# Performance work log

Measured on AMD Instinct MI355X. Metric: run time of the kernel, lower is better.

Reference implementation:

```python
import jax, jax.numpy as jnp
import numpy as np

V = 25426          # tgt_vocab_size
D = 256            # d_model
H = 8              # heads
DH = 2048          # dim_head (d_ff passed positionally as d_head in source)
INNER = H * DH     # 16384
CLS = V            # cls token id (same value for t1 and t2 in source)
MASK_TOK = V + 2   # mask token id
VT = V + 3         # total embedding vocab


def _pos_encoding(n, d):
    pos = np.arange(n, dtype=np.float32)[:, None]
    div = np.exp(np.arange(0, d, 2, dtype=np.float32) * (-np.log(10000.0) / d))
    pe = np.zeros((n, d), dtype=np.float32)
    pe[:, 0::2] = np.sin(pos * div)
    pe[:, 1::2] = np.cos(pos * div)
    return jnp.asarray(pe)


def _layernorm(x, g, b, eps=1e-5):
    m = x.mean(-1, keepdims=True)
    v = ((x - m) ** 2).mean(-1, keepdims=True)
    return (x - m) / jnp.sqrt(v + eps) * g + b


def _cross_attn(x, ctx, pad_mask, Wq, Wk, Wv, Wo, bo):
    # x: [B,N,D], ctx: [B,M,Dc], pad_mask: [B,M] True = masked
    B, N, _ = x.shape
    M = ctx.shape[1]
    scale = DH ** -0.5
    q = (x @ Wq).reshape(B, N, H, DH)
    k = (ctx @ Wk).reshape(B, M, H, DH)
    v = (ctx @ Wv).reshape(B, M, H, DH)
    sim = jnp.einsum('bihd,bjhd->bhij', q, k) * scale  # [B,H,N,M]
    neg = -jnp.finfo(sim.dtype).max
    sim = jnp.where(pad_mask[:, None, None, :], neg, sim)
    attn = jax.nn.softmax(sim, axis=-1)
    out = jnp.einsum('bhij,bjhd->bihd', attn, v).reshape(B, N, INNER)
    return out @ Wo + bo


def _decoder(x, tgt_pad, src_mask, enc_output, p):
    a = _cross_attn(x, x, tgt_pad, p['Wq_s'], p['Wk_s'], p['Wv_s'], p['Wo_s'], p['bo_s'])
    x = _layernorm(x + a, p['g1'], p['be1'])
    a = _cross_attn(x, enc_output, src_mask, p['Wq_c'], p['Wk_c'], p['Wv_c'], p['Wo_c'], p['bo_c'])
    x = _layernorm(x + a, p['g2'], p['be2'])
    f = jax.nn.gelu(x @ p['W1'] + p['b1'], approximate=False) @ p['W2'] + p['b2']
    x = _layernorm(x + f, p['g3'], p['be3'])
    return x


def setup_inputs() -> dict:
    key = jax.random.key(0)
    ks = jax.random.split(key, 32)
    B, S, L = 2, 1024, 767
    d = {
        'src_input_id': jax.random.randint(ks[0], (B, S), 0, V),
        'tgt_input_id_t1': jax.random.randint(ks[1], (B, L), 0, V),
        'tgt_input_id_t2': jax.random.randint(ks[2], (B, L), 0, V),
        'original_lens': jax.random.randint(ks[3], (B,), 1, L),
        'enc_output': jax.random.normal(ks[4], (B, S, D), dtype=jnp.float32),
    }
    emb = jax.random.normal(ks[5], (VT, D), dtype=jnp.float32) * 0.02
    d['token_emb'] = emb.at[0].set(0.0)  # padding_idx=0
    s = 0.02
    d['Wq_s'] = jax.random.normal(ks[6], (D, INNER)) * s
    d['Wk_s'] = jax.random.normal(ks[7], (D, INNER)) * s
    d['Wv_s'] = jax.random.normal(ks[8], (D, INNER)) * s
    d['Wo_s'] = jax.random.normal(ks[9], (INNER, D)) * s
    d['bo_s'] = jnp.zeros((D,), jnp.float32)
    d['Wq_c'] = jax.random.normal(ks[10], (D, INNER)) * s
    d['Wk_c'] = jax.random.normal(ks[11], (D, INNER)) * s
    d['Wv_c'] = jax.random.normal(ks[12], (D, INNER)) * s
    d['Wo_c'] = jax.random.normal(ks[13], (INNER, D)) * s
    d['bo_c'] = jnp.zeros((D,), jnp.float32)
    d['W1'] = jax.random.normal(ks[14], (D, D)) * s  # Mlp hidden collapses to D (source bug)
    d['b1'] = jnp.zeros((D,), jnp.float32)
    d['W2'] = jax.random.normal(ks[15], (D, D)) * s
    d['b2'] = jnp.zeros((D,), jnp.float32)
    for i, n in enumerate(['g1', 'g2', 'g3']):
        d[n] = jnp.ones((D,), jnp.float32)
    for n in ['be1', 'be2', 'be3']:
        d[n] = jnp.zeros((D,), jnp.float32)
    d['Wfc'] = jax.random.normal(ks[16], (D, V)) * s
    d['bfc'] = jnp.zeros((V,), jnp.float32)
    return d


def reference(src_input_id, tgt_input_id_t1, tgt_input_id_t2, original_lens,
              enc_output, token_emb,
              Wq_s, Wk_s, Wv_s, Wo_s, bo_s,
              Wq_c, Wk_c, Wv_c, Wo_c, bo_c,
              W1, b1, W2, b2, g1, be1, g2, be2, g3, be3, Wfc, bfc):
    p = dict(Wq_s=Wq_s, Wk_s=Wk_s, Wv_s=Wv_s, Wo_s=Wo_s, bo_s=bo_s,
             Wq_c=Wq_c, Wk_c=Wk_c, Wv_c=Wv_c, Wo_c=Wo_c, bo_c=bo_c,
             W1=W1, b1=b1, W2=W2, b2=b2, g1=g1, be1=be1, g2=g2, be2=be2, g3=g3, be3=be3)
    B = tgt_input_id_t1.shape[0]
    cls = jnp.full((B, 1), CLS, dtype=tgt_input_id_t1.dtype)
    t1 = jnp.concatenate([cls, tgt_input_id_t1], axis=1)
    t2 = jnp.concatenate([cls, tgt_input_id_t2], axis=1)
    tgt = jnp.concatenate([t1, t2], axis=1)          # [B, T]
    tgt_pad = tgt == 0
    src_mask = src_input_id == 0
    # generate=True path: mask positions where id==mask_token or id==0
    tgt_mask = (tgt == MASK_TOK) | (tgt == 0)
    tgt_ids = jnp.where(tgt_mask, MASK_TOK, tgt)
    x = token_emb[tgt_ids]                            # [B, T, D]
    pe = _pos_encoding(x.shape[1], D)
    x = 2.0 * x + pe[None, :, :]                      # prepare_tokens: x + (x + pe), faithful to source
    x = _decoder(x, tgt_pad, src_mask, enc_output, p)
    logits = x @ Wfc + bfc
    return logits[:, 1:, :], x[:, 0, :]
```

## Files before the change

### kernel.cpp

```cpp
#include <hip/hip_runtime.h>
#include <hip/hip_bf16.h>
#include <float.h>
#include <math.h>

#define BB 2
#define SS 1024
#define LL 767
#define TT 1536
#define DD 256
#define HH 8
#define DHD 2048
#define INNER_ 16384
#define VV 25426
#define VPAD 25472
#define CLS_TOK 25426
#define MASK_TOKEN 25428
#define ROWS (BB*TT)
#define SROWS (BB*SS)

typedef __attribute__((ext_vector_type(8))) __bf16 bf16x8;
typedef __attribute__((ext_vector_type(4))) float f32x4;

__device__ __forceinline__ unsigned short f2bu(float f) {
    union { float f; unsigned u; } v; v.f = f;
    unsigned r = v.u + 0x7fff + ((v.u >> 16) & 1);
    return (unsigned short)(r >> 16);
}
__device__ __forceinline__ float bu2f(unsigned short u) {
    union { unsigned u; float f; } v; v.u = ((unsigned)u) << 16;
    return v.f;
}

__device__ __forceinline__ void gload16(const void* g, void* l) {
    __builtin_amdgcn_global_load_lds(
        (const __attribute__((address_space(1))) void*)g,
        (__attribute__((address_space(3))) void*)l, 16, 0, 0);
}


__global__ __launch_bounds__(256) void embed_kernel(
    const int* __restrict__ t1, const int* __restrict__ t2,
    const float* __restrict__ emb, float* __restrict__ x,
    unsigned short* __restrict__ xb, unsigned char* __restrict__ tgt_pad)
{
    int t = blockIdx.x, b = blockIdx.y, d = threadIdx.x;
    int raw;
    if (t == 0)            raw = CLS_TOK;
    else if (t <= LL)      raw = t1[b * LL + (t - 1)];
    else if (t == LL + 1)  raw = CLS_TOK;
    else                   raw = t2[b * LL + (t - LL - 2)];
    int id = (raw == 0 || raw == MASK_TOKEN) ? MASK_TOKEN : raw;
    int i = d >> 1;
    float ang = (float)t * expf(-0.03597789208f * (float)(2 * i));
    float pe = (d & 1) ? cosf(ang) : sinf(ang);
    float val = 2.f * emb[(long long)id * DD + d] + pe;
    long long idx = ((long long)(b * TT + t)) * DD + d;
    x[idx] = val;
    xb[idx] = f2bu(val);
    if (d == 0) tgt_pad[b * TT + t] = (raw == 0) ? 1 : 0;
}

__global__ __launch_bounds__(256) void masks_kernel(
    const int* __restrict__ src, unsigned char* __restrict__ m, int* __restrict__ rm)
{
    int i = blockIdx.x * 256 + threadIdx.x;
    if (i < SROWS) m[i] = (src[i] == 0) ? 1 : 0;
    if (i < ROWS) {
        int b = i / TT, t = i % TT;
        rm[i] = (t == 0) ? -1 : (b * (TT - 1) + t - 1);
    }
}

__global__ __launch_bounds__(256) void copycls_kernel(
    const float* __restrict__ x, float* __restrict__ out2)
{
    int b = blockIdx.x, d = threadIdx.x;
    out2[b * DD + d] = x[(long long)b * TT * DD + d];
}

__global__ __launch_bounds__(256) void conv_bf16v4(
    const float* __restrict__ in, unsigned short* __restrict__ out)
{
    size_t i = ((size_t)blockIdx.x * 256 + threadIdx.x) * 4;
    float4 v = *reinterpret_cast<const float4*>(in + i);
    ushort4 u;
    u.x = f2bu(v.x); u.y = f2bu(v.y); u.z = f2bu(v.z); u.w = f2bu(v.w);
    *reinterpret_cast<ushort4*>(out + i) = u;
}

__global__ __launch_bounds__(256) void convW6(
    const float* __restrict__ w0, const float* __restrict__ w1,
    const float* __restrict__ w2, const float* __restrict__ w3,
    const float* __restrict__ w4, const float* __restrict__ w5,
    unsigned short* __restrict__ dst)
{
    int seg = blockIdx.y;
    const float* s = seg == 0 ? w0 : seg == 1 ? w1 : seg == 2 ? w2 :
                     seg == 3 ? w3 : seg == 4 ? w4 : w5;
    size_t i = ((size_t)blockIdx.x * 256 + threadIdx.x) * 4;
    float4 v = *reinterpret_cast<const float4*>(s + i);
    ushort4 u;
    u.x = f2bu(v.x); u.y = f2bu(v.y); u.z = f2bu(v.z); u.w = f2bu(v.w);
    *reinterpret_cast<ushort4*>(dst + (size_t)seg * ((size_t)DD * INNER_) + i) = u;
}

__global__ __launch_bounds__(256) void transpose_conv(
    const float* __restrict__ in, unsigned short* __restrict__ out,
    int R, int Cin, int Nout)
{
    __shared__ float t[32][33];
    int k0 = blockIdx.x * 32, n0 = blockIdx.y * 32;
#pragma unroll
    for (int i = 0; i < 4; ++i) {
        int k = k0 + threadIdx.y + i * 8;
        int n = n0 + threadIdx.x;
        t[threadIdx.y + i * 8][threadIdx.x] = (n < Cin) ? in[(size_t)k * Cin + n] : 0.f;
    }
    __syncthreads();
#pragma unroll
    for (int i = 0; i < 4; ++i) {
        int n = n0 + threadIdx.y + i * 8;
        int k = k0 + threadIdx.x;
        out[(size_t)n * R + k] = f2bu(t[threadIdx.x][threadIdx.y + i * 8]);
    }
}

template<int STORE, int SPLITK>
__global__ __launch_bounds__(256) void gemm_bt(
    const unsigned short* __restrict__ A, int lda,
    const unsigned short* __restrict__ B, int ldb,
    void* __restrict__ Cv, int ldc,
    int M, int N, int K, float alpha, int zs,
    long long sAb, long long sAh, long long sBb, long long sBh,
    long long sCb, long long sCh,
    const float* __restrict__ bias, const int* __restrict__ rowmap)
{
    __shared__ unsigned short As[8192];
    __shared__ unsigned short Bs[8192];
    const int tid = threadIdx.x;
    const int w = tid >> 6, l = tid & 63;
    const int m0 = blockIdx.x * 128, n0 = blockIdx.y * 128;

    int kbeg = 0, kend = K;
    long long czoff = 0;
    if (SPLITK > 1) {
        constexpr int KSH = (SPLITK == 8) ? 3 : (SPLITK == 4) ? 2 : (SPLITK == 2) ? 1 : 0;
        int kidx = blockIdx.z & (SPLITK - 1);
        int zr = blockIdx.z >> KSH;
        int zb = zr >> zs;
        int zh = zr - (zb << zs);
        int kc = K / SPLITK;
        kbeg = kidx * kc; kend = kbeg + kc;
        A += zb * sAb + zh * sAh;
        B += zb * sBb + zh * sBh;
        czoff = zb * sCb + zh * sCh;
    } else {
        int zb = blockIdx.z >> zs;
        int zh = blockIdx.z - (zb << zs);
        A += zb * sAb + zh * sAh;
        B += zb * sBb + zh * sBh;
        czoff = zb * sCb + zh * sCh;
    }

    const int wr = (w >> 1) << 6, wc = (w & 1) << 6;
    const int lrow = l & 15, lk = l >> 4;

    const int sro = (w << 3) + (l >> 3);
    const int sko = (((l & 7) ^ (l >> 3)) << 3);
    const int ldst = (w << 10) + (l << 4);

    f32x4 acc[4][4];
#pragma unroll
    for (int mi = 0; mi < 4; ++mi)
#pragma unroll
        for (int ni = 0; ni < 4; ++ni)
            acc[mi][ni] = (f32x4){0.f, 0.f, 0.f, 0.f};

    for (int kt = kbeg; kt < kend; kt += 64) {
#pragma unroll
        for (int j = 0; j < 4; ++j)
            gload16(A + (size_t)(m0 + sro + j * 32) * lda + kt + sko,
                    (char*)As + (j << 12) + ldst);
#pragma unroll
        for (int j = 0; j < 4; ++j)
            gload16(B + (size_t)(n0 + sro + j * 32) * ldb + kt + sko,
                    (char*)Bs + (j << 12) + ldst);
        __syncthreads();

#pragma unroll
        for (int kk = 0; kk < 2; ++kk) {
            const int slot = (kk << 2) + lk;
            bf16x8 af[4], bfr[4];
#pragma unroll
            for (int mi = 0; mi < 4; ++mi) {
                int ra = wr + (mi << 4) + lrow;
                af[mi] = *reinterpret_cast<const bf16x8*>(
                    (const char*)As + (ra << 7) + ((slot ^ (ra & 7)) << 4));
            }
#pragma unroll
            for (int ni = 0; ni < 4; ++ni) {
                int rb = wc + (ni << 4) + lrow;
                bfr[ni] = *reinterpret_cast<const bf16x8*>(
                    (const char*)Bs + (rb << 7) + ((slot ^ (rb & 7)) << 4));
            }
#pragma unroll
            for (int mi = 0; mi < 4; ++mi)
#pragma unroll
                for (int ni = 0; ni < 4; ++ni)
                    acc[mi][ni] = __builtin_amdgcn_mfma_f32_16x16x32_bf16(
                        af[mi], bfr[ni], acc[mi][ni], 0, 0, 0);
        }
        __syncthreads();
    }

    if (STORE == 0) {
        unsigned short* C = (unsigned short*)Cv + czoff;
#pragma unroll
        for (int mi = 0; mi < 4; ++mi) {
            int r = m0 + wr + (mi << 4) + (lk << 2);
#pragma unroll
            for (int ni = 0; ni < 4; ++ni) {
                int c = n0 + wc + (ni << 4) + lrow;
#pragma unroll
                for (int q = 0; q < 4; ++q)
                    C[(size_t)(r + q) * ldc + c] = f2bu(acc[mi][ni][q] * alpha);
            }
        }
    } else if (STORE == 1) {
        unsigned short* C = (unsigned short*)Cv + czoff;
#pragma unroll
        for (int ni = 0; ni < 4; ++ni) {
            int c = n0 + wc + (ni << 4) + lrow;
#pragma unroll
            for (int mi = 0; mi < 4; ++mi) {
                int r = m0 + wr + (mi << 4) + (lk << 2);
                ushort4 u;
                u.x = f2bu(acc[mi][ni][0] * alpha);
                u.y = f2bu(acc[mi][ni][1] * alpha);
                u.z = f2bu(acc[mi][ni][2] * alpha);
                u.w = f2bu(acc[mi][ni][3] * alpha);
                *reinterpret_cast<ushort4*>(&C[(size_t)c * ldc + r]) = u;
            }
        }
    } else if (STORE == 2) {
        float* C = (float*)Cv;
#pragma unroll
        for (int mi = 0; mi < 4; ++mi) {
            int r = m0 + wr + (mi << 4) + (lk << 2);
#pragma unroll
            for (int q = 0; q < 4; ++q) {
                int rm = rowmap[r + q];
                if (rm < 0) continue;
#pragma unroll
                for (int ni = 0; ni < 4; ++ni) {
                    int c = n0 + wc + (ni << 4) + lrow;
                    if (c < N) C[(size_t)rm * ldc + c] = acc[mi][ni][q] * alpha + bias[c];
                }
            }
        }
    } else if (STORE == 3) {
        float* C = (float*)Cv + czoff;
#pragma unroll
        for (int mi = 0; mi < 4; ++mi) {
            int r = m0 + wr + (mi << 4) + (lk << 2);
#pragma unroll
            for (int ni = 0; ni < 4; ++ni) {
                int c = n0 + wc + (ni << 4) + lrow;
#pragma unroll
                for (int q = 0; q < 4; ++q)
                    atomicAdd(&C[(size_t)(r + q) * ldc + c], acc[mi][ni][q] * alpha);
            }
        }
    } else if (STORE == 4) {
        unsigned short* C = (unsigned short*)Cv + czoff;
#pragma unroll
        for (int mi = 0; mi < 4; ++mi) {
            int r = m0 + wr + (mi << 4) + (lk << 2);
#pragma unroll
            for (int ni = 0; ni < 4; ++ni) {
                int c = n0 + wc + (ni << 4) + lrow;
#pragma unroll
                for (int q = 0; q < 4; ++q) {
                    float v = acc[mi][ni][q] * alpha + bias[c];
                    v = 0.5f * v * (1.f + erff(v * 0.70710678118f));
                    C[(size_t)(r + q) * ldc + c] = f2bu(v);
                }
            }
        }
    } else if (STORE == 5) {
        float* C = (float*)Cv + czoff;
#pragma unroll
        for (int mi = 0; mi < 4; ++mi) {
            int r = m0 + wr + (mi << 4) + (lk << 2);
#pragma unroll
            for (int ni = 0; ni < 4; ++ni) {
                int c = n0 + wc + (ni << 4) + lrow;
#pragma unroll
                for (int q = 0; q < 4; ++q)
                    C[(size_t)(r + q) * ldc + c] = acc[mi][ni][q] * alpha;
            }
        }
    } else if (STORE == 6) {
        unsigned short* C = (unsigned short*)Cv + czoff;
        const unsigned char* mrow =
            (const unsigned char*)rowmap + (size_t)(blockIdx.z >> zs) * N;
        float* rsum = (float*)bias;
        float rpart[4][4];
#pragma unroll
        for (int mi = 0; mi < 4; ++mi)
#pragma unroll
            for (int q = 0; q < 4; ++q) rpart[mi][q] = 0.f;
#pragma unroll
        for (int mi = 0; mi < 4; ++mi) {
            int r = m0 + wr + (mi << 4) + (lk << 2);
#pragma unroll
            for (int ni = 0; ni < 4; ++ni) {
                int c = n0 + wc + (ni << 4) + lrow;
                bool msk = mrow[c] != 0;
#pragma unroll
                for (int q = 0; q < 4; ++q) {
                    float e = msk ? 0.f : expf(acc[mi][ni][q] * alpha);
                    C[(size_t)(r + q) * ldc + c] = f2bu(e);
                    rpart[mi][q] += e;
                }
            }
        }
#pragma unroll
        for (int mi = 0; mi < 4; ++mi)
#pragma unroll
            for (int q = 0; q < 4; ++q) {
                float s = rpart[mi][q];
                s += __shfl_xor(s, 1);
                s += __shfl_xor(s, 2);
                s += __shfl_xor(s, 4);
                s += __shfl_xor(s, 8);
                if (lrow == 0) {
                    int r = m0 + wr + (mi << 4) + (lk << 2) + q;
                    atomicAdd(&rsum[(size_t)blockIdx.z * M + r], s);
                }
            }
    } else {
        float* C = (float*)Cv + czoff;
#pragma unroll
        for (int mi = 0; mi < 4; ++mi) {
            int r = m0 + wr + (mi << 4) + (lk << 2);
#pragma unroll
            for (int q = 0; q < 4; ++q) {
                float rinv = 1.f / bias[(size_t)blockIdx.z * M + r + q];
#pragma unroll
                for (int ni = 0; ni < 4; ++ni) {
                    int c = n0 + wc + (ni << 4) + lrow;
                    atomicAdd(&C[(size_t)(r + q) * ldc + c], acc[mi][ni][q] * rinv);
                }
            }
        }
    }
}

__global__ __launch_bounds__(256) void ln_kernel(
    float* __restrict__ x, const float* __restrict__ a,
    const float* __restrict__ abias,
    const float* __restrict__ g, const float* __restrict__ be,
    unsigned short* __restrict__ xb)
{
    __shared__ float red[4];
    const long long r = blockIdx.x;
    const int d = threadIdx.x;
    const long long idx = r * DD + d;
    float v = x[idx] + a[idx];
    if (abias) v += abias[d];

    float s = v;
#pragma unroll
    for (int off = 32; off > 0; off >>= 1) s += __shfl_down(s, off);
    if ((d & 63) == 0) red[d >> 6] = s;
    __syncthreads();
    float mean = (red[0] + red[1] + red[2] + red[3]) * (1.f / DD);
    __syncthreads();

    float df = v - mean;
    float s2 = df * df;
#pragma unroll
    for (int off = 32; off > 0; off >>= 1) s2 += __shfl_down(s2, off);
    if ((d & 63) == 0) red[d >> 6] = s2;
    __syncthreads();
    float var = (red[0] + red[1] + red[2] + red[3]) * (1.f / DD);

    float o = df / sqrtf(var + 1e-5f) * g[d] + be[d];
    x[idx] = o;
    xb[idx] = f2bu(o);
}

extern "C" void kernel_launch(void* const* d_in, const int* in_sizes, int n_in,
                              void* d_out, int out_size, void* d_ws, size_t ws_size,
                              hipStream_t stream)
{
    const int*   src_ids = (const int*)d_in[0];
    const int*   t1      = (const int*)d_in[1];
    const int*   t2      = (const int*)d_in[2];
    const float* enc  = (const float*)d_in[4];
    const float* emb  = (const float*)d_in[5];
    const float* Wq_s = (const float*)d_in[6];
    const float* Wk_s = (const float*)d_in[7];
    const float* Wv_s = (const float*)d_in[8];
    const float* Wo_s = (const float*)d_in[9];
    const float* bo_s = (const float*)d_in[10];
    const float* Wq_c = (const float*)d_in[11];
    const float* Wk_c = (const float*)d_in[12];
    const float* Wv_c = (const float*)d_in[13];
    const float* Wo_c = (const float*)d_in[14];
    const float* bo_c = (const float*)d_in[15];
    const float* W1   = (const float*)d_in[16];
    const float* b1   = (const float*)d_in[17];
    const float* W2   = (const float*)d_in[18];
    const float* b2   = (const float*)d_in[19];
    const float* g1   = (const float*)d_in[20];
    const float* g2v  = (const float*)d_in[21];
    const float* g3   = (const float*)d_in[22];
    const float* be1  = (const float*)d_in[23];
    const float* be2  = (const float*)d_in[24];
    const float* be3  = (const float*)d_in[25];
    const float* Wfc  = (const float*)d_in[26];
    const float* bfc  = (const float*)d_in[27];

    char* p = (char*)d_ws;
    float* x    = (float*)p;           p += (size_t)ROWS * DD * 4;
    float* aout = (float*)p;           p += (size_t)ROWS * DD * 4;
    float* rsum = (float*)p;           p += (size_t)16 * TT * 4;
    unsigned short* h1b  = (unsigned short*)p; p += (size_t)ROWS * DD * 2;
    unsigned short* xb   = (unsigned short*)p; p += (size_t)ROWS * DD * 2;
    unsigned short* encb = (unsigned short*)p; p += (size_t)SROWS * DD * 2;
    unsigned short* Wqb_s = (unsigned short*)p; p += (size_t)DD * INNER_ * 2;
    unsigned short* Wkb_s = (unsigned short*)p; p += (size_t)DD * INNER_ * 2;
    unsigned short* Wvb_s = (unsigned short*)p; p += (size_t)DD * INNER_ * 2;
    unsigned short* Wqb_c = (unsigned short*)p; p += (size_t)DD * INNER_ * 2;
    unsigned short* Wkb_c = (unsigned short*)p; p += (size_t)DD * INNER_ * 2;
    unsigned short* Wvb_c = (unsigned short*)p; p += (size_t)DD * INNER_ * 2;
    unsigned short* WoTs  = (unsigned short*)p; p += (size_t)DD * INNER_ * 2;
    unsigned short* WoTc  = (unsigned short*)p; p += (size_t)DD * INNER_ * 2;
    unsigned short* WfcT  = (unsigned short*)p; p += (size_t)VPAD * DD * 2;
    unsigned short* W1Tb  = (unsigned short*)p; p += (size_t)DD * DD * 2;
    unsigned short* W2Tb  = (unsigned short*)p; p += (size_t)DD * DD * 2;
    unsigned short* MtNb  = (unsigned short*)p; p += (size_t)4 * 524288 * 2;
    unsigned char* tgtpad = (unsigned char*)p; p += ROWS;
    unsigned char* srcpad = (unsigned char*)p; p += SROWS;
    p = (char*)(((size_t)p + 15) & ~(size_t)15);
    int* rowmap = (int*)p;             p += (size_t)ROWS * 4;

    unsigned short* Mtb_s = MtNb;
    unsigned short* Ntb_s = MtNb + 524288;
    unsigned short* Mtb_c = MtNb + 2 * 524288;
    unsigned short* Ntb_c = MtNb + 3 * 524288;

    unsigned short* ob = (unsigned short*)d_out;
    unsigned short* simS = ob;
    unsigned short* Pb   = ob + 37748736;
    unsigned short* YTb  = Pb + 6291456;
    float* MNacc = (float*)d_out;

    const size_t accset = (size_t)ROWS * DD * 4 + (size_t)16 * TT * 4;
    const long long WBLK = 4194304;

    embed_kernel<<<dim3(TT, BB), 256, 0, stream>>>(t1, t2, emb, x, xb, tgtpad);
    masks_kernel<<<dim3(ROWS / 256), 256, 0, stream>>>(src_ids, srcpad, rowmap);
    conv_bf16v4<<<dim3((SROWS * DD) / 1024), 256, 0, stream>>>(enc, encb);

    dim3 tcb(32, 8);
    convW6<<<dim3((DD * INNER_) / 1024, 6), 256, 0, stream>>>(
        Wq_s, Wk_s, Wv_s, Wq_c, Wk_c, Wv_c, Wqb_s);
    transpose_conv<<<dim3(512, 8), tcb, 0, stream>>>(Wo_s, WoTs, INNER_, DD, DD);
    transpose_conv<<<dim3(512, 8), tcb, 0, stream>>>(Wo_c, WoTc, INNER_, DD, DD);
    transpose_conv<<<dim3(8, VPAD / 32), tcb, 0, stream>>>(Wfc, WfcT, DD, VV, VPAD);
    transpose_conv<<<dim3(8, 8), tcb, 0, stream>>>(W1, W1Tb, DD, DD, DD);
    transpose_conv<<<dim3(8, 8), tcb, 0, stream>>>(W2, W2Tb, DD, DD, DD);

    const float scale = 0.022097086912079608f;
    const long long Z0 = 0;

    hipMemsetAsync(MNacc, 0, (size_t)4 * 524288 * 4, stream);
    gemm_bt<3, 4><<<dim3(2, 2, 64), 256, 0, stream>>>(
        Wkb_s, INNER_, Wqb_s, INNER_, MNacc, 256, 256, 256, DHD, 1.f, 3,
        3 * WBLK, 2048, 3 * WBLK, 2048, 2 * 524288, 65536, nullptr, nullptr);
    gemm_bt<3, 4><<<dim3(2, 2, 64), 256, 0, stream>>>(
        WoTs, INNER_, Wvb_s, INNER_, MNacc + 524288, 2048, 256, 256, DHD, 1.f, 3,
        WBLK, 2048, 3 * WBLK, 2048, 2 * 524288, 256, nullptr, nullptr);
    conv_bf16v4<<<dim3((4 * 524288) / 1024), 256, 0, stream>>>(MNacc, MtNb);

    hipMemsetAsync(aout, 0, accset, stream);
    gemm_bt<0, 1><<<dim3(24, 2, 8), 256, 0, stream>>>(
        xb, DD, Mtb_s, DD, Pb, DD, ROWS, DD, DD, 1.f, 3,
        Z0, Z0, Z0, 65536, Z0, 786432, nullptr, nullptr);
    gemm_bt<1, 1><<<dim3(24, 2, 8), 256, 0, stream>>>(
        xb, DD, Ntb_s, 2048, YTb, ROWS, ROWS, DD, DD, 1.f, 3,
        Z0, Z0, Z0, 256, Z0, 786432, nullptr, nullptr);
    gemm_bt<6, 1><<<dim3(12, 12, 16), 256, 0, stream>>>(
        Pb, DD, xb, DD, simS, TT, TT, TT, DD, scale, 3,
        393216, 786432, 393216, Z0,
        18874368, 2359296, (const float*)rsum, (const int*)tgtpad);
    gemm_bt<7, 1><<<dim3(12, 2, 16), 256, 0, stream>>>(
        simS, TT, YTb, ROWS, aout, DD, TT, DD, TT, 1.f, 3,
        18874368, 2359296, 1536, 786432,
        393216, Z0, rsum, nullptr);
    ln_kernel<<<dim3(ROWS), 256, 0, stream>>>(x, aout, bo_s, g1, be1, xb);

    hipMemsetAsync(aout, 0, accset, stream);
    gemm_bt<0, 1><<<dim3(24, 2, 8), 256, 0, stream>>>(
        xb, DD, Mtb_c, DD, Pb, DD, ROWS, DD, DD, 1.f, 3,
        Z0, Z0, Z0, 65536, Z0, 786432, nullptr, nullptr);
    gemm_bt<1, 1><<<dim3(16, 2, 8), 256, 0, stream>>>(
        encb, DD, Ntb_c, 2048, YTb, SROWS, SROWS, DD, DD, 1.f, 3,
        Z0, Z0, Z0, 256, Z0, 524288, nullptr, nullptr);
    gemm_bt<6, 1><<<dim3(12, 8, 16), 256, 0, stream>>>(
        Pb, DD, encb, DD, simS, SS, TT, SS, DD, scale, 3,
        393216, 786432, 262144, Z0,
        12582912, 1572864, (const float*)rsum, (const int*)srcpad);
    gemm_bt<7, 1><<<dim3(12, 2, 16), 256, 0, stream>>>(
        simS, SS, YTb, SROWS, aout, DD, TT, DD, SS, 1.f, 3,
        12582912, 1572864, 1024, 524288,
        393216, Z0, rsum, nullptr);
    ln_kernel<<<dim3(ROWS), 256, 0, stream>>>(x, aout, bo_c, g2v, be2, xb);

    gemm_bt<4, 1><<<dim3(24, 2, 1), 256, 0, stream>>>(
        xb, DD, W1Tb, DD, h1b, DD, ROWS, DD, DD, 1.f, 0,
        Z0, Z0, Z0, Z0, Z0, Z0, b1, nullptr);
    gemm_bt<5, 1><<<dim3(24, 2, 1), 256, 0, stream>>>(
        h1b, DD, W2Tb, DD, aout, DD, ROWS, DD, DD, 1.f, 0,
        Z0, Z0, Z0, Z0, Z0, Z0, nullptr, nullptr);
    ln_kernel<<<dim3(ROWS), 256, 0, stream>>>(x, aout, b2, g3, be3, xb);

    gemm_bt<2, 1><<<dim3(24, VPAD / 128, 1), 256, 0, stream>>>(
        xb, DD, WfcT, DD, d_out, VV, ROWS, VV, DD, 1.f, 0,
        Z0, Z0, Z0, Z0, Z0, Z0, bfc, rowmap);

    copycls_kernel<<<dim3(BB), 256, 0, stream>>>(
        x, (float*)d_out + (long long)BB * (TT - 1) * VV);
}
```

Baseline: 566.9 us.

## Fuse attention score, exp and value GEMMs into one flash-style kernel

Replaces the separate score GEMM (writing exp'd bf16 scores to global memory with atomic row sums) and the value GEMM (atomic float accumulation across heads) with a single kernel. It keeps the query tile in LDS, streams key/value tiles, computes unnormalized exp scores in LDS, and accumulates the output per head. Per-head outputs are written without atomics and summed in a new layernorm kernel, which removes the memsets and the large intermediate score tensor. Softmax still skips max subtraction, as before, and the kernel uses about 66KB of LDS per block. Its 384-block grid may underfill the GPU.

```diff
diff --git a/kernel.cpp b/kernel.cpp
--- a/kernel.cpp
+++ b/kernel.cpp
@@ -287,7 +287,7 @@
                 }
             }
         }
-    } else if (STORE == 5) {
+    } else {
         float* C = (float*)Cv + czoff;
 #pragma unroll
         for (int mi = 0; mi < 4; ++mi) {
@@ -300,61 +300,187 @@
                     C[(size_t)(r + q) * ldc + c] = acc[mi][ni][q] * alpha;
             }
         }
-    } else if (STORE == 6) {
-        unsigned short* C = (unsigned short*)Cv + czoff;
-        const unsigned char* mrow =
-            (const unsigned char*)rowmap + (size_t)(blockIdx.z >> zs) * N;
-        float* rsum = (float*)bias;
-        float rpart[4][4];
-#pragma unroll
-        for (int mi = 0; mi < 4; ++mi)
-#pragma unroll
-            for (int q = 0; q < 4; ++q) rpart[mi][q] = 0.f;
+    }
+}
+
+template<int KVT>
+__global__ __launch_bounds__(256) void attn_fused(
+    const unsigned short* __restrict__ P,
+    const unsigned short* __restrict__ KV,
+    const unsigned short* __restrict__ YT,
+    float* __restrict__ Oh,
+    const unsigned char* __restrict__ mask,
+    float scale)
+{
+    constexpr int kvtok = KVT * 64;
+    constexpr int ytld = BB * kvtok;
+    __shared__ unsigned short Pq[64 * 256];
+    __shared__ unsigned short Stg[64 * 256];
+    __shared__ unsigned short Sc[64 * 64];
+    __shared__ float rs[64];
+
+    const int tid = threadIdx.x;
+    const int w = tid >> 6, l = tid & 63;
+    const int lrow = l & 15, lk = l >> 4;
+    const int q0 = blockIdx.x * 64;
+    const int z = blockIdx.y;
+    const int b = z >> 3, h = z & 7;
+
+    if (tid < 64) rs[tid] = 0.f;
+
+    const unsigned short* Prow = P + ((size_t)h * 3072 + b * 1536 + q0) * 256;
+#pragma unroll
+    for (int rdx = 0; rdx < 8; ++rdx) {
+        int ob = rdx * 4096 + tid * 16;
+        int row = ob >> 9;
+        int sl = (ob >> 4) & 31;
+        gload16(Prow + (size_t)row * 256 + (sl ^ (row & 7)) * 8, (char*)Pq + ob);
+    }
+    const unsigned char* mp = mask + b * kvtok;
+    const unsigned short* kvp = KV + (size_t)b * kvtok * 256;
+    const unsigned short* ytp = YT + (size_t)h * 256 * ytld + (size_t)b * kvtok;
+
+    f32x4 acc[4][4];
+#pragma unroll
+    for (int mi = 0; mi < 4; ++mi)
+#pragma unroll
+        for (int ni = 0; ni < 4; ++ni)
+            acc[mi][ni] = (f32x4){0.f, 0.f, 0.f, 0.f};
+
+    for (int kt = 0; kt < KVT; ++kt) {
+#pragma unroll
+        for (int rdx = 0; rdx < 8; ++rdx) {
+            int ob = rdx * 4096 + tid * 16;
+            int row = ob >> 9;
+            int sl = (ob >> 4) & 31;
+            gload16(kvp + (size_t)(kt * 64 + row) * 256 + (sl ^ (row & 7)) * 8,
+                    (char*)Stg + ob);
+        }
+        __syncthreads();
+
+        f32x4 sacc[4];
+#pragma unroll
+        for (int mi = 0; mi < 4; ++mi) sacc[mi] = (f32x4){0.f, 0.f, 0.f, 0.f};
+#pragma unroll
+        for (int kk = 0; kk < 8; ++kk) {
+            int brow = w * 16 + lrow;
+            bf16x8 bfr = *reinterpret_cast<const bf16x8*>(
+                (const char*)Stg + brow * 512 + (((kk << 2) + lk) ^ (brow & 7)) * 16);
+#pragma unroll
+            for (int mi = 0; mi < 4; ++mi) {
+                int arow = mi * 16 + lrow;
+                bf16x8 af = *reinterpret_cast<const bf16x8*>(
+                    (const char*)Pq + arow * 512 + (((kk << 2) + lk) ^ (arow & 7)) * 16);
+                sacc[mi] = __builtin_amdgcn_mfma_f32_16x16x32_bf16(af, bfr, sacc[mi], 0, 0, 0);
+            }
+        }
+        const int colL = w * 16 + lrow;
+        const bool mk = mp[kt * 64 + colL] != 0;
 #pragma unroll
         for (int mi = 0; mi < 4; ++mi) {
-            int r = m0 + wr + (mi << 4) + (lk << 2);
-#pragma unroll
-            for (int ni = 0; ni < 4; ++ni) {
-                int c = n0 + wc + (ni << 4) + lrow;
-                bool msk = mrow[c] != 0;
-#pragma unroll
-                for (int q = 0; q < 4; ++q) {
-                    float e = msk ? 0.f : expf(acc[mi][ni][q] * alpha);
-                    C[(size_t)(r + q) * ldc + c] = f2bu(e);
-                    rpart[mi][q] += e;
-                }
-            }
-        }
-#pragma unroll
-        for (int mi = 0; mi < 4; ++mi)
 #pragma unroll
             for (int q = 0; q < 4; ++q) {
-                float s = rpart[mi][q];
+                int row = mi * 16 + (lk << 2) + q;
+                float e = mk ? 0.f : expf(sacc[mi][q] * scale);
+                int byt = row * 128 + (((colL >> 3) ^ (row & 7)) << 4) + (colL & 7) * 2;
+                *reinterpret_cast<unsigned short*>((char*)Sc + byt) = f2bu(e);
+                float s = e;
                 s += __shfl_xor(s, 1);
                 s += __shfl_xor(s, 2);
                 s += __shfl_xor(s, 4);
                 s += __shfl_xor(s, 8);
-                if (lrow == 0) {
-                    int r = m0 + wr + (mi << 4) + (lk << 2) + q;
-                    atomicAdd(&rsum[(size_t)blockIdx.z * M + r], s);
-                }
-            }
-    } else {
-        float* C = (float*)Cv + czoff;
-#pragma unroll
-        for (int mi = 0; mi < 4; ++mi) {
-            int r = m0 + wr + (mi << 4) + (lk << 2);
-#pragma unroll
-            for (int q = 0; q < 4; ++q) {
-                float rinv = 1.f / bias[(size_t)blockIdx.z * M + r + q];
-#pragma unroll
-                for (int ni = 0; ni < 4; ++ni) {
-                    int c = n0 + wc + (ni << 4) + lrow;
-                    atomicAdd(&C[(size_t)(r + q) * ldc + c], acc[mi][ni][q] * rinv);
-                }
-            }
-        }
-    }
+                if (lrow == 0) atomicAdd(&rs[row], s);
+            }
+        }
+        __syncthreads();
+
+#pragma unroll
+        for (int rdx = 0; rdx < 8; ++rdx) {
+            int ob = rdx * 4096 + tid * 16;
+            int row = ob >> 7;
+            int sl = (ob >> 4) & 7;
+            gload16(ytp + (size_t)row * ytld + kt * 64 + (sl ^ (row & 7)) * 8,
+                    (char*)Stg + ob);
+        }
+        __syncthreads();
+
+#pragma unroll
+        for (int kk = 0; kk < 2; ++kk) {
+            bf16x8 af[4], bfr[4];
+#pragma unroll
+            for (int mi = 0; mi < 4; ++mi) {
+                int ar = mi * 16 + lrow;
+                af[mi] = *reinterpret_cast<const bf16x8*>(
+                    (const char*)Sc + ar * 128 + (((kk << 2) + lk) ^ (ar & 7)) * 16);
+            }
+#pragma unroll
+            for (int ni = 0; ni < 4; ++ni) {
+                int br = w * 64 + ni * 16 + lrow;
+                bfr[ni] = *reinterpret_cast<const bf16x8*>(
+                    (const char*)Stg + br * 128 + (((kk << 2) + lk) ^ (br & 7)) * 16);
+            }
+#pragma unroll
+            for (int mi = 0; mi < 4; ++mi)
+#pragma unroll
+                for (int ni = 0; ni < 4; ++ni)
+                    acc[mi][ni] = __builtin_amdgcn_mfma_f32_16x16x32_bf16(
+                        af[mi], bfr[ni], acc[mi][ni], 0, 0, 0);
+        }
+        __syncthreads();
+    }
+
+    float* op = Oh + (size_t)z * (1536 * 256) + (size_t)q0 * 256;
+#pragma unroll
+    for (int mi = 0; mi < 4; ++mi) {
+#pragma unroll
+        for (int q = 0; q < 4; ++q) {
+            int row = mi * 16 + (lk << 2) + q;
+            float rinv = 1.f / rs[row];
+#pragma unroll
+            for (int ni = 0; ni < 4; ++ni) {
+                int col = w * 64 + ni * 16 + lrow;
+                op[(size_t)row * 256 + col] = acc[mi][ni][q] * rinv;
+            }
+        }
+    }
+}
+
+__global__ __launch_bounds__(256) void ln8_kernel(
+    float* __restrict__ x, const float* __restrict__ Oh,
+    const float* __restrict__ abias,
+    const float* __restrict__ g, const float* __restrict__ be,
+    unsigned short* __restrict__ xb)
+{
+    __shared__ float red[4];
+    const int r = blockIdx.x;
+    const int b = (r >= 1536) ? 1 : 0;
+    const int t = r - b * 1536;
+    const int d = threadIdx.x;
+    const long long idx = (long long)r * DD + d;
+    float v = x[idx] + abias[d];
+    const float* op = Oh + ((size_t)b * 8 * 1536 + t) * 256 + d;
+#pragma unroll
+    for (int h = 0; h < 8; ++h) v += op[(size_t)h * 1536 * 256];
+
+    float s = v;
+#pragma unroll
+    for (int off = 32; off > 0; off >>= 1) s += __shfl_down(s, off);
+    if ((d & 63) == 0) red[d >> 6] = s;
+    __syncthreads();
+    float mean = (red[0] + red[1] + red[2] + red[3]) * (1.f / DD);
+    __syncthreads();
+
+    float df = v - mean;
+    float s2 = df * df;
+#pragma unroll
+    for (int off = 32; off > 0; off >>= 1) s2 += __shfl_down(s2, off);
+    if ((d & 63) == 0) red[d >> 6] = s2;
+    __syncthreads();
+    float var = (red[0] + red[1] + red[2] + red[3]) * (1.f / DD);
+
+    float o = df / sqrtf(var + 1e-5f) * g[d] + be[d];
+    x[idx] = o;
+    xb[idx] = f2bu(o);
 }
 
 __global__ __launch_bounds__(256) void ln_kernel(
@@ -426,7 +552,6 @@
     char* p = (char*)d_ws;
     float* x    = (float*)p;           p += (size_t)ROWS * DD * 4;
     float* aout = (float*)p;           p += (size_t)ROWS * DD * 4;
-    float* rsum = (float*)p;           p += (size_t)16 * TT * 4;
     unsigned short* h1b  = (unsigned short*)p; p += (size_t)ROWS * DD * 2;
     unsigned short* xb   = (unsigned short*)p; p += (size_t)ROWS * DD * 2;
     unsigned short* encb = (unsigned short*)p; p += (size_t)SROWS * DD * 2;
@@ -452,13 +577,12 @@
     unsigned short* Mtb_c = MtNb + 2 * 524288;
     unsigned short* Ntb_c = MtNb + 3 * 524288;
 
-    unsigned short* ob = (unsigned short*)d_out;
-    unsigned short* simS = ob;
-    unsigned short* Pb   = ob + 37748736;
-    unsigned short* YTb  = Pb + 6291456;
+    float* Oh = (float*)d_out;
+    unsigned short* ob16 = (unsigned short*)d_out;
+    unsigned short* Pb  = ob16 + 12582912;
+    unsigned short* YTb = Pb + 6291456;
     float* MNacc = (float*)d_out;
 
-    const size_t accset = (size_t)ROWS * DD * 4 + (size_t)16 * TT * 4;
     const long long WBLK = 4194304;
 
     embed_kernel<<<dim3(TT, BB), 256, 0, stream>>>(t1, t2, emb, x, xb, tgtpad);
@@ -486,39 +610,25 @@
         WBLK, 2048, 3 * WBLK, 2048, 2 * 524288, 256, nullptr, nullptr);
     conv_bf16v4<<<dim3((4 * 524288) / 1024), 256, 0, stream>>>(MNacc, MtNb);
 
-    hipMemsetAsync(aout, 0, accset, stream);
     gemm_bt<0, 1><<<dim3(24, 2, 8), 256, 0, stream>>>(
         xb, DD, Mtb_s, DD, Pb, DD, ROWS, DD, DD, 1.f, 3,
         Z0, Z0, Z0, 65536, Z0, 786432, nullptr, nullptr);
     gemm_bt<1, 1><<<dim3(24, 2, 8), 256, 0, stream>>>(
         xb, DD, Ntb_s, 2048, YTb, ROWS, ROWS, DD, DD, 1.f, 3,
         Z0, Z0, Z0, 256, Z0, 786432, nullptr, nullptr);
-    gemm_bt<6, 1><<<dim3(12, 12, 16), 256, 0, stream>>>(
-        Pb, DD, xb, DD, simS, TT, TT, TT, DD, scale, 3,
-        393216, 786432, 393216, Z0,
-        18874368, 2359296, (const float*)rsum, (const int*)tgtpad);
-    gemm_bt<7, 1><<<dim3(12, 2, 16), 256, 0, stream>>>(
-        simS, TT, YTb, ROWS, aout, DD, TT, DD, TT, 1.f, 3,
-        18874368, 2359296, 1536, 786432,
-        393216, Z0, rsum, nullptr);
-    ln_kernel<<<dim3(ROWS), 256, 0, stream>>>(x, aout, bo_s, g1, be1, xb);
-
-    hipMemsetAsync(aout, 0, accset, stream);
+    attn_fused<24><<<dim3(24, 16), 256, 0, stream>>>(
+        Pb, xb, YTb, Oh, tgtpad, scale);
+    ln8_kernel<<<dim3(ROWS), 256, 0, stream>>>(x, Oh, bo_s, g1, be1, xb);
+
     gemm_bt<0, 1><<<dim3(24, 2, 8), 256, 0, stream>>>(
         xb, DD, Mtb_c, DD, Pb, DD, ROWS, DD, DD, 1.f, 3,
         Z0, Z0, Z0, 65536, Z0, 786432, nullptr, nullptr);
     gemm_bt<1, 1><<<dim3(16, 2, 8), 256, 0, stream>>>(
         encb, DD, Ntb_c, 2048, YTb, SROWS, SROWS, DD, DD, 1.f, 3,
         Z0, Z0, Z0, 256, Z0, 524288, nullptr, nullptr);
-    gemm_bt<6, 1><<<dim3(12, 8, 16), 256, 0, stream>>>(
-        Pb, DD, encb, DD, simS, SS, TT, SS, DD, scale, 3,
-        393216, 786432, 262144, Z0,
-        12582912, 1572864, (const float*)rsum, (const int*)srcpad);
-    gemm_bt<7, 1><<<dim3(12, 2, 16), 256, 0, stream>>>(
-        simS, SS, YTb, SROWS, aout, DD, TT, DD, SS, 1.f, 3,
-        12582912, 1572864, 1024, 524288,
-        393216, Z0, rsum, nullptr);
-    ln_kernel<<<dim3(ROWS), 256, 0, stream>>>(x, aout, bo_c, g2v, be2, xb);
+    attn_fused<16><<<dim3(24, 16), 256, 0, stream>>>(
+        Pb, encb, YTb, Oh, srcpad, scale);
+    ln8_kernel<<<dim3(ROWS), 256, 0, stream>>>(x, Oh, bo_c, g2v, be2, xb);
 
     gemm_bt<4, 1><<<dim3(24, 2, 1), 256, 0, stream>>>(
         xb, DD, W1Tb, DD, h1b, DD, ROWS, DD, DD, 1.f, 0,
```

New measurement: 628.0 us. 1.11x slower.
